# Kernel optimization log

Measured on AMD Instinct MI355X. Metric: run time of the kernel, lower is better.

Reference implementation:

```python
import jax, jax.numpy as jnp
import numpy as np

N_NODES = 100000
N_EDGES = 1600000
NFEAT = 128
NHID = 128
NCLS = 40


def _glorot(key, shape):
    fan_in, fan_out = shape[1], shape[0]
    lim = (6.0 / (fan_in + fan_out)) ** 0.5
    return jax.random.uniform(key, shape, jnp.float32, -lim, lim)


def setup_inputs() -> dict:
    key = jax.random.key(0)
    ks = jax.random.split(key, 10)
    x = jax.random.normal(ks[0], (N_NODES, NFEAT), jnp.float32)
    edge_index = jax.random.randint(ks[1], (2, N_EDGES), 0, N_NODES, jnp.int64)
    return {
        "x": x,
        "edge_index": edge_index,
        # SAGEConv layer 0: lin_l (neighbor aggr, with bias) and lin_r (root)
        "W_l0": _glorot(ks[2], (NHID, NFEAT)),
        "b_l0": jnp.zeros((NHID,), jnp.float32),
        "W_r0": _glorot(ks[3], (NHID, NFEAT)),
        # SAGEConv layer 1
        "W_l1": _glorot(ks[4], (NHID, NHID)),
        "b_l1": jnp.zeros((NHID,), jnp.float32),
        "W_r1": _glorot(ks[5], (NHID, NHID)),
        # classifier
        "W_cls": _glorot(ks[6], (NCLS, NHID)),
        "b_cls": jnp.zeros((NCLS,), jnp.float32),
    }


def _sage_conv(x, src, dst, deg_inv, W_l, b_l, W_r):
    # gather source-node features along edges, mean-aggregate at targets
    msgs = x[src]                                            # [E, d_in]
    aggr = jax.ops.segment_sum(msgs, dst, num_segments=N_NODES)  # [N, d_in]
    aggr = aggr * deg_inv[:, None]                           # mean
    # out = lin_l(aggr) + lin_r(x)
    return aggr @ W_l.T + b_l + x @ W_r.T


def reference(x, edge_index, W_l0, b_l0, W_r0, W_l1, b_l1, W_r1, W_cls, b_cls):
    src, dst = edge_index[0], edge_index[1]
    deg = jax.ops.segment_sum(jnp.ones((src.shape[0],), x.dtype), dst,
                              num_segments=N_NODES)
    deg_inv = 1.0 / jnp.maximum(deg, 1.0)

    h = jax.nn.relu(_sage_conv(x, src, dst, deg_inv, W_l0, b_l0, W_r0))
    h = jax.nn.relu(_sage_conv(h, src, dst, deg_inv, W_l1, b_l1, W_r1))
    return h @ W_cls.T + b_cls  # [N, ncls]
```

## Files before the change

kernel.cpp:

```cpp
#include <hip/hip_runtime.h>

#define NN 100000
#define NE 1600000
#define DD 128
#define NCLS_ 40
#define PAD 64
#define NPART 8
#define PSZ 12500
#define PBLK 250
#define ECHUNK 6400
#define NITER 25

typedef unsigned short u16;
typedef unsigned int u32;
typedef __attribute__((ext_vector_type(2))) unsigned int u32x2;
typedef __attribute__((ext_vector_type(8))) short short8;
typedef __attribute__((ext_vector_type(4))) float f32x4;

static __device__ __forceinline__ u16 f2b(float f) {
  u32 u = __float_as_uint(f);
  u32 r = (u + 0x7FFFu + ((u >> 16) & 1u)) >> 16;
  return (u16)r;
}

__global__ void k_flag(const int* __restrict__ ei, int* __restrict__ flag) {
  __shared__ int nz;
  if (threadIdx.x == 0) nz = 0;
  __syncthreads();
  if (threadIdx.x < 512) {
    int w = ei[2 * threadIdx.x + 1];
    if (w != 0) atomicOr(&nz, 1);
  }
  __syncthreads();
  if (threadIdx.x == 0) flag[0] = (nz == 0) ? 1 : 0;
}

static __device__ __forceinline__ int eget_nt(const int* ei, int pos, int is64) {
  return is64 ? __builtin_nontemporal_load(ei + 2 * (size_t)pos)
              : __builtin_nontemporal_load(ei + pos);
}

static __device__ __forceinline__ void cvt1(const float* __restrict__ s,
                                            u16* __restrict__ d, int j) {
  float4 v;
  v.x = __builtin_nontemporal_load((const float*)s + 4 * (size_t)j + 0);
  v.y = __builtin_nontemporal_load((const float*)s + 4 * (size_t)j + 1);
  v.z = __builtin_nontemporal_load((const float*)s + 4 * (size_t)j + 2);
  v.w = __builtin_nontemporal_load((const float*)s + 4 * (size_t)j + 3);
  u32x2 pk;
  pk.x = (u32)f2b(v.x) | ((u32)f2b(v.y) << 16);
  pk.y = (u32)f2b(v.z) | ((u32)f2b(v.w) << 16);
  __builtin_nontemporal_store(pk, (u32x2*)d + j);
}

__global__ __launch_bounds__(256) void k_prep(
    const int* __restrict__ ei, const int* __restrict__ flag,
    int* __restrict__ cnt, int* __restrict__ csrp,
    const float* __restrict__ x, u16* __restrict__ xb,
    const float* __restrict__ w0, const float* __restrict__ w1,
    const float* __restrict__ w2, const float* __restrict__ w3,
    u16* __restrict__ o0, u16* __restrict__ o1,
    u16* __restrict__ o2, u16* __restrict__ o3,
    const float* __restrict__ wc, u16* __restrict__ wcb) {
  int is64 = flag[0];
  int g = blockIdx.x & (NPART - 1);
  int sub = blockIdx.x >> 3;
  int e0 = sub * ECHUNK;
  int lo = g * PSZ;
  int gtid = blockIdx.x * 256 + threadIdx.x;
#pragma unroll 1
  for (int it = 0; it < NITER; ++it) {
    int e = e0 + it * 256 + threadIdx.x;
    int dst = eget_nt(ei, NE + e, is64);
    if ((u32)(dst - lo) < (u32)PSZ) {
      int src = eget_nt(ei, e, is64);
      int r = atomicAdd(&cnt[dst], 1);
      if (r < PAD) csrp[dst * PAD + r] = src;
    }
    if (it < 7) {
      int i = it * 512000 + gtid;
      if (i < NN * DD / 4) cvt1(x, xb, i);
    } else if (it == 7) {
      if (gtid < 4 * 4096) {
        int which = gtid >> 12, j = gtid & 4095;
        const float* s = which == 0 ? w0 : which == 1 ? w1 : which == 2 ? w2 : w3;
        u16* d = which == 0 ? o0 : which == 1 ? o1 : which == 2 ? o2 : o3;
        cvt1(s, d, j);
      } else if (gtid < 4 * 4096 + 6144) {
        int i = gtid - 4 * 4096;
        float v = (i < NCLS_ * DD) ? wc[i] : 0.f;
        wcb[i] = f2b(v);
      }
    }
  }
}

template <bool LAST>
__global__ __launch_bounds__(256, 2) void k_fused(
    const u16* __restrict__ in, const int* __restrict__ csrp,
    const int* __restrict__ cnt,
    const u16* __restrict__ WL, const u16* __restrict__ WR,
    const float* __restrict__ bias,
    u16* __restrict__ hout,
    const u16* __restrict__ Wc, const float* __restrict__ bc,
    float* __restrict__ out) {
  __shared__ u32 agt[16 * 64];
  __shared__ u32 h1t[LAST ? 16 * 64 : 1];
  int wv = threadIdx.x >> 6;
  int lane = threadIdx.x & 63;
  int l16 = lane & 15;
  int base16 = blockIdx.x * 16;
  const u32* in32 = (const u32*)in;

  for (int j = 0; j < 4; j++) {
    int nl = wv * 4 + j;
    int wid = base16 + nl;
    int deg = cnt[wid];
    int nb = deg > PAD ? PAD : deg;
    const int* seg = csrp + (size_t)wid * PAD;
    float a0 = 0.f, a1 = 0.f;
    int full = nb >> 4;
    for (int b = 0; b < full; b++) {
      int c = seg[b * 16 + l16];
      u32 v[16];
#pragma unroll
      for (int k = 0; k < 16; k++) {
        int sk = __builtin_amdgcn_readlane(c, k);
        v[k] = in32[(size_t)sk * 64 + lane];
      }
#pragma unroll
      for (int k = 0; k < 16; k++) {
        a0 += __uint_as_float(v[k] << 16);
        a1 += __uint_as_float(v[k] & 0xFFFF0000u);
      }
    }
    int done = full << 4;
    int rem = nb - done;
    if (rem) {
      int c = seg[done + (l16 < rem ? l16 : 0)];
      u32 v[16];
#pragma unroll
      for (int k = 0; k < 16; k++) {
        if (k < rem) {
          int sk = __builtin_amdgcn_readlane(c, k);
          v[k] = in32[(size_t)sk * 64 + lane];
        }
      }
#pragma unroll
      for (int k = 0; k < 16; k++) {
        if (k < rem) {
          a0 += __uint_as_float(v[k] << 16);
          a1 += __uint_as_float(v[k] & 0xFFFF0000u);
        }
      }
    }
    float sc = 1.0f / (float)(deg > 1 ? deg : 1);
    u32 pk = (u32)f2b(a0 * sc) | ((u32)f2b(a1 * sc) << 16);
    agt[nl * 64 + (lane ^ ((nl & 7) << 2))] = pk;
  }
  __syncthreads();

  int m = lane & 15, kg = lane >> 4;
  f32x4 acc[2];
#pragma unroll
  for (int t = 0; t < 2; t++) acc[t] = (f32x4){0.f, 0.f, 0.f, 0.f};
#pragma unroll
  for (int kk = 0; kk < 4; kk++) {
    int ko = kk * 32 + kg * 8;
    int cu = (ko >> 1) ^ ((m & 7) << 2);
    short8 aA = *(const short8*)((const u16*)agt + m * 128 + cu * 2);
    short8 aX = *(const short8*)(in + (size_t)(base16 + m) * DD + ko);
#pragma unroll
    for (int tt = 0; tt < 2; tt++) {
      int t = wv * 2 + tt;
      short8 bL = *(const short8*)(WL + (size_t)(t * 16 + m) * DD + ko);
      acc[tt] = __builtin_amdgcn_mfma_f32_16x16x32_bf16(aA, bL, acc[tt], 0, 0, 0);
      short8 bR = *(const short8*)(WR + (size_t)(t * 16 + m) * DD + ko);
      acc[tt] = __builtin_amdgcn_mfma_f32_16x16x32_bf16(aX, bR, acc[tt], 0, 0, 0);
    }
  }
#pragma unroll
  for (int tt = 0; tt < 2; tt++) {
    int o = (wv * 2 + tt) * 16 + m;
#pragma unroll
    for (int r = 0; r < 4; r++) {
      int nl = kg * 4 + r;
      float v = fmaxf(acc[tt][r] + bias[o], 0.f);
      if constexpr (!LAST) {
        hout[(size_t)(base16 + nl) * DD + o] = f2b(v);
      } else {
        ((u16*)h1t)[nl * 128 + (o ^ ((nl & 7) << 3))] = f2b(v);
      }
    }
  }

  if constexpr (LAST) {
    __syncthreads();
    if (wv == 0) {
      f32x4 ac[3];
#pragma unroll
      for (int t = 0; t < 3; t++) ac[t] = (f32x4){0.f, 0.f, 0.f, 0.f};
#pragma unroll
      for (int kk = 0; kk < 4; kk++) {
        int ko = kk * 32 + kg * 8;
        int cu = (ko >> 1) ^ ((m & 7) << 2);
        short8 aH = *(const short8*)((const u16*)h1t + m * 128 + cu * 2);
#pragma unroll
        for (int t = 0; t < 3; t++) {
          short8 bC = *(const short8*)(Wc + (size_t)(t * 16 + m) * DD + ko);
          ac[t] = __builtin_amdgcn_mfma_f32_16x16x32_bf16(aH, bC, ac[t], 0, 0, 0);
        }
      }
#pragma unroll
      for (int t = 0; t < 3; t++) {
        int o = t * 16 + m;
        if (o < NCLS_) {
#pragma unroll
          for (int r = 0; r < 4; r++) {
            int node = base16 + kg * 4 + r;
            out[(size_t)node * NCLS_ + o] = ac[t][r] + bc[o];
          }
        }
      }
    }
  }
}

extern "C" void kernel_launch(void* const* d_in, const int* in_sizes, int n_in,
                              void* d_out, int out_size, void* d_ws, size_t ws_size,
                              hipStream_t stream) {
  const float* x = (const float*)d_in[0];
  const int* ei = (const int*)d_in[1];
  const float* wl0 = (const float*)d_in[2];
  const float* bl0 = (const float*)d_in[3];
  const float* wr0 = (const float*)d_in[4];
  const float* wl1 = (const float*)d_in[5];
  const float* bl1 = (const float*)d_in[6];
  const float* wr1 = (const float*)d_in[7];
  const float* wcls = (const float*)d_in[8];
  const float* bcls = (const float*)d_in[9];

  char* ws = (char*)d_ws;
  size_t off = 0;
  auto alloc = [&](size_t b) {
    size_t r = off;
    off += (b + 255) & ~(size_t)255;
    return r;
  };
  int* flag = (int*)(ws + alloc(4));
  int* cnt = (int*)(ws + alloc((size_t)NN * 4));
  int* csrp = (int*)(ws + alloc((size_t)NN * PAD * 4));
  u16* xb = (u16*)(ws + alloc((size_t)NN * DD * 2));
  u16* h0 = (u16*)(ws + alloc((size_t)NN * DD * 2));
  u16* wl0b = (u16*)(ws + alloc((size_t)DD * DD * 2));
  u16* wr0b = (u16*)(ws + alloc((size_t)DD * DD * 2));
  u16* wl1b = (u16*)(ws + alloc((size_t)DD * DD * 2));
  u16* wr1b = (u16*)(ws + alloc((size_t)DD * DD * 2));
  u16* wclsb = (u16*)(ws + alloc((size_t)48 * DD * 2));
  if (off > ws_size) return;

  (void)hipMemsetAsync(cnt, 0, (size_t)NN * 4, stream);
  k_flag<<<1, 512, 0, stream>>>(ei, flag);
  k_prep<<<NPART * PBLK, 256, 0, stream>>>(ei, flag, cnt, csrp,
                                           x, xb, wl0, wr0, wl1, wr1,
                                           wl0b, wr0b, wl1b, wr1b, wcls, wclsb);

  const int FB = NN / 16;

  k_fused<false><<<FB, 256, 0, stream>>>(xb, csrp, cnt, wl0b, wr0b, bl0,
                                         h0, nullptr, nullptr, nullptr);
  k_fused<true><<<FB, 256, 0, stream>>>(h0, csrp, cnt, wl1b, wr1b, bl1,
                                        nullptr, wclsb, bcls, (float*)d_out);
}
```

Baseline: 306.2 us.

## Give each wavefront its own 16-node tile to remove block barriers

Each wavefront now aggregates all 16 nodes of its own tile and computes the full 128-wide output with 8 MFMA accumulators. Previously a block of four waves shared one 16-node tile, split the output columns across waves and synchronised with __syncthreads. This removes the barriers and the serial classifier stage that only wave 0 ran, so waves no longer wait for each other. In exchange each wave reloads all weight rows, uses more accumulator registers and more LDS per block, and there are four times fewer blocks.

```diff
diff --git a/kernel.cpp b/kernel.cpp
--- a/kernel.cpp
+++ b/kernel.cpp
@@ -104,17 +104,17 @@
     u16* __restrict__ hout,
     const u16* __restrict__ Wc, const float* __restrict__ bc,
     float* __restrict__ out) {
-  __shared__ u32 agt[16 * 64];
-  __shared__ u32 h1t[LAST ? 16 * 64 : 1];
+  __shared__ u32 tile[4][16 * 64];
   int wv = threadIdx.x >> 6;
   int lane = threadIdx.x & 63;
   int l16 = lane & 15;
-  int base16 = blockIdx.x * 16;
+  int nbase = blockIdx.x * 64 + wv * 16;
+  if (nbase >= NN) return;
+  u32* T = tile[wv];
   const u32* in32 = (const u32*)in;
 
-  for (int j = 0; j < 4; j++) {
-    int nl = wv * 4 + j;
-    int wid = base16 + nl;
+  for (int nl = 0; nl < 16; nl++) {
+    int wid = nbase + nl;
     int deg = cnt[wid];
     int nb = deg > PAD ? PAD : deg;
     const int* seg = csrp + (size_t)wid * PAD;
@@ -156,70 +156,65 @@
     }
     float sc = 1.0f / (float)(deg > 1 ? deg : 1);
     u32 pk = (u32)f2b(a0 * sc) | ((u32)f2b(a1 * sc) << 16);
-    agt[nl * 64 + (lane ^ ((nl & 7) << 2))] = pk;
-  }
-  __syncthreads();
+    T[nl * 64 + (lane ^ ((nl & 7) << 2))] = pk;
+  }
 
   int m = lane & 15, kg = lane >> 4;
-  f32x4 acc[2];
-#pragma unroll
-  for (int t = 0; t < 2; t++) acc[t] = (f32x4){0.f, 0.f, 0.f, 0.f};
+  f32x4 acc[8];
+#pragma unroll
+  for (int t = 0; t < 8; t++) acc[t] = (f32x4){0.f, 0.f, 0.f, 0.f};
 #pragma unroll
   for (int kk = 0; kk < 4; kk++) {
     int ko = kk * 32 + kg * 8;
     int cu = (ko >> 1) ^ ((m & 7) << 2);
-    short8 aA = *(const short8*)((const u16*)agt + m * 128 + cu * 2);
-    short8 aX = *(const short8*)(in + (size_t)(base16 + m) * DD + ko);
-#pragma unroll
-    for (int tt = 0; tt < 2; tt++) {
-      int t = wv * 2 + tt;
+    short8 aA = *(const short8*)((const u16*)T + m * 128 + cu * 2);
+    short8 aX = *(const short8*)(in + (size_t)(nbase + m) * DD + ko);
+#pragma unroll
+    for (int t = 0; t < 8; t++) {
       short8 bL = *(const short8*)(WL + (size_t)(t * 16 + m) * DD + ko);
-      acc[tt] = __builtin_amdgcn_mfma_f32_16x16x32_bf16(aA, bL, acc[tt], 0, 0, 0);
+      acc[t] = __builtin_amdgcn_mfma_f32_16x16x32_bf16(aA, bL, acc[t], 0, 0, 0);
       short8 bR = *(const short8*)(WR + (size_t)(t * 16 + m) * DD + ko);
-      acc[tt] = __builtin_amdgcn_mfma_f32_16x16x32_bf16(aX, bR, acc[tt], 0, 0, 0);
-    }
-  }
-#pragma unroll
-  for (int tt = 0; tt < 2; tt++) {
-    int o = (wv * 2 + tt) * 16 + m;
+      acc[t] = __builtin_amdgcn_mfma_f32_16x16x32_bf16(aX, bR, acc[t], 0, 0, 0);
+    }
+  }
+#pragma unroll
+  for (int t = 0; t < 8; t++) {
+    int o = t * 16 + m;
 #pragma unroll
     for (int r = 0; r < 4; r++) {
       int nl = kg * 4 + r;
-      float v = fmaxf(acc[tt][r] + bias[o], 0.f);
+      float v = fmaxf(acc[t][r] + bias[o], 0.f);
       if constexpr (!LAST) {
-        hout[(size_t)(base16 + nl) * DD + o] = f2b(v);
+        hout[(size_t)(nbase + nl) * DD + o] = f2b(v);
       } else {
-        ((u16*)h1t)[nl * 128 + (o ^ ((nl & 7) << 3))] = f2b(v);
+        ((u16*)T)[nl * 128 + (o ^ ((nl & 7) << 3))] = f2b(v);
       }
     }
   }
 
   if constexpr (LAST) {
-    __syncthreads();
-    if (wv == 0) {
-      f32x4 ac[3];
-#pragma unroll
-      for (int t = 0; t < 3; t++) ac[t] = (f32x4){0.f, 0.f, 0.f, 0.f};
-#pragma unroll
-      for (int kk = 0; kk < 4; kk++) {
-        int ko = kk * 32 + kg * 8;
-        int cu = (ko >> 1) ^ ((m & 7) << 2);
-        short8 aH = *(const short8*)((const u16*)h1t + m * 128 + cu * 2);
-#pragma unroll
-        for (int t = 0; t < 3; t++) {
-          short8 bC = *(const short8*)(Wc + (size_t)(t * 16 + m) * DD + ko);
-          ac[t] = __builtin_amdgcn_mfma_f32_16x16x32_bf16(aH, bC, ac[t], 0, 0, 0);
-        }
-      }
+    f32x4 ac[3];
+#pragma unroll
+    for (int t = 0; t < 3; t++) ac[t] = (f32x4){0.f, 0.f, 0.f, 0.f};
+#pragma unroll
+    for (int kk = 0; kk < 4; kk++) {
+      int ko = kk * 32 + kg * 8;
+      int cu = (ko >> 1) ^ ((m & 7) << 2);
+      short8 aH = *(const short8*)((const u16*)T + m * 128 + cu * 2);
 #pragma unroll
       for (int t = 0; t < 3; t++) {
-        int o = t * 16 + m;
-        if (o < NCLS_) {
-#pragma unroll
-          for (int r = 0; r < 4; r++) {
-            int node = base16 + kg * 4 + r;
-            out[(size_t)node * NCLS_ + o] = ac[t][r] + bc[o];
-          }
+        short8 bC = *(const short8*)(Wc + (size_t)(t * 16 + m) * DD + ko);
+        ac[t] = __builtin_amdgcn_mfma_f32_16x16x32_bf16(aH, bC, ac[t], 0, 0, 0);
+      }
+    }
+#pragma unroll
+    for (int t = 0; t < 3; t++) {
+      int o = t * 16 + m;
+      if (o < NCLS_) {
+#pragma unroll
+        for (int r = 0; r < 4; r++) {
+          int node = nbase + kg * 4 + r;
+          out[(size_t)node * NCLS_ + o] = ac[t][r] + bc[o];
         }
       }
     }
@@ -265,7 +260,7 @@
                                            x, xb, wl0, wr0, wl1, wr1,
                                            wl0b, wr0b, wl1b, wr1b, wcls, wclsb);
 
-  const int FB = NN / 16;
+  const int FB = (NN + 63) / 64;
 
   k_fused<false><<<FB, 256, 0, stream>>>(xb, csrp, cnt, wl0b, wr0b, bl0,
                                          h0, nullptr, nullptr, nullptr);
```

Result: slower. 338.1 us (+10.4%).
